# Optimization experiments

Measured on AMD Instinct MI355X. Metric: run time of the kernel, lower is better.

Reference implementation:

```python
import jax, jax.numpy as jnp
import numpy as np
from jax.ops import segment_sum, segment_max

N, E, F, H, G, P, C = 50000, 600000, 128, 128, 64, 32, 10
HEADS = 3
BN_EPS = 1e-5
COS_EPS = 1e-8


def setup_inputs() -> dict:
    key = jax.random.key(0)
    ks = jax.random.split(key, 32)
    rn = lambda k, shape, s: jax.random.normal(k, shape, jnp.float32) * s
    inp = {
        "x": jax.random.normal(ks[0], (N, F), jnp.float32),
        "edge_index": jax.random.randint(ks[1], (2, E), 0, N, jnp.int32),
        "batch": jnp.sort(jax.random.randint(ks[2], (N,), 0, G, jnp.int32)),
        # GCNConv
        "W1": rn(ks[3], (F, H), F ** -0.5), "b1": jnp.zeros((H,), jnp.float32),
        # SAGEConv (lin_l on aggregated neighbors, lin_r on root)
        "Wl": rn(ks[4], (H, H), H ** -0.5), "Wr": rn(ks[5], (H, H), H ** -0.5),
        "bs": jnp.zeros((H,), jnp.float32),
        # GATConv, heads=3, concat=False
        "Wg": rn(ks[6], (H, HEADS * H), H ** -0.5),
        "a_src": rn(ks[7], (HEADS, H), H ** -0.5),
        "a_dst": rn(ks[8], (HEADS, H), H ** -0.5),
        "bg": jnp.zeros((H,), jnp.float32),
        # prototype head / classifier / decoder
        "protos": jax.random.normal(ks[9], (P, H), jnp.float32),
        "Wc": rn(ks[10], (H, C), H ** -0.5), "bc": jnp.zeros((C,), jnp.float32),
        "Wd1": rn(ks[11], (H, 2 * H), H ** -0.5), "bd1": jnp.zeros((2 * H,), jnp.float32),
        "Wd2": rn(ks[12], (2 * H, F), (2 * H) ** -0.5), "bd2": jnp.zeros((F,), jnp.float32),
    }
    # BatchNorm (eval mode): gamma, beta, running mean/var for bn1..bn3
    for i in range(3):
        k0, k1, k2 = jax.random.split(ks[13 + i], 3)
        inp[f"g{i+1}"] = 1.0 + rn(k0, (H,), 0.05)
        inp[f"be{i+1}"] = rn(k1, (H,), 0.05)
        inp[f"m{i+1}"] = rn(k2, (H,), 0.1)
        inp[f"v{i+1}"] = jnp.ones((H,), jnp.float32)
    return inp


def _bn(x, g, b, m, v):
    return (x - m) * jax.lax.rsqrt(v + BN_EPS) * g + b


def _forward(x, edge_index, batch,
             W1, b1, g1, be1, m1, v1,
             Wl, Wr, bs, g2, be2, m2, v2,
             Wg, a_src, a_dst, bg, g3, be3, m3, v3,
             protos, Wc, bc, Wd1, bd1, Wd2, bd2):
    src, dst = edge_index[0], edge_index[1]
    ones_e = jnp.ones((src.shape[0],), x.dtype)

    # --- GCNConv: symmetric norm with self-loops ---
    h = x @ W1                                        # [N, H]
    deg = segment_sum(ones_e, dst, num_segments=N) + 1.0
    dinv = jax.lax.rsqrt(deg)
    coef = dinv[src] * dinv[dst]                      # [E]
    h1 = segment_sum(h[src] * coef[:, None], dst, num_segments=N)
    h1 = h1 + h * (dinv * dinv)[:, None] + b1         # self-loop term + bias
    h1 = jax.nn.elu(_bn(h1, g1, be1, m1, v1))         # dropout = identity (eval)

    # --- SAGEConv: mean aggregation (no self-loops) ---
    cnt = segment_sum(ones_e, dst, num_segments=N)
    mean_nb = segment_sum(h1[src], dst, num_segments=N) / jnp.maximum(cnt, 1.0)[:, None]
    h2 = mean_nb @ Wl + h1 @ Wr + bs
    h2 = jax.nn.elu(_bn(h2, g2, be2, m2, v2))

    # --- GATConv: heads=3, concat=False (mean), with self-loops ---
    hg = (h2 @ Wg).reshape(N, HEADS, H)               # [N, 3, H]
    al_src = jnp.einsum('nhf,hf->nh', hg, a_src)      # [N, 3]
    al_dst = jnp.einsum('nhf,hf->nh', hg, a_dst)
    loop = jnp.arange(N, dtype=src.dtype)
    s2 = jnp.concatenate([src, loop])
    d2 = jnp.concatenate([dst, loop])
    e = jax.nn.leaky_relu(al_src[s2] + al_dst[d2], 0.2)   # [E+N, 3]
    emax = segment_max(e, d2, num_segments=N)             # every node has a self-loop
    ex = jnp.exp(e - emax[d2])
    den = segment_sum(ex, d2, num_segments=N)
    alpha = ex / den[d2]                                  # [E+N, 3]
    h3 = segment_sum(hg[s2] * alpha[:, :, None], d2, num_segments=N)
    h3 = h3.mean(axis=1) + bg                             # concat=False -> head mean
    h3 = jax.nn.elu(_bn(h3, g3, be3, m3, v3))

    # --- global mean pool over graphs ---
    gcnt = segment_sum(jnp.ones((N,), x.dtype), batch, num_segments=G)
    pooled = segment_sum(h3, batch, num_segments=G) / jnp.maximum(gcnt, 1.0)[:, None]

    # --- prototype head: cosine sim -> softmax -> mix ---
    xn = pooled / jnp.maximum(jnp.linalg.norm(pooled, axis=-1, keepdims=True), COS_EPS)
    pn = protos / jnp.maximum(jnp.linalg.norm(protos, axis=-1, keepdims=True), COS_EPS)
    sims = xn @ pn.T                                      # [G, P]
    assignments = jax.nn.softmax(sims, axis=-1)
    proto_emb = assignments @ protos                      # [G, H]
    logits = proto_emb @ Wc + bc                          # [G, C]
    reconstructed = jax.nn.relu(pooled @ Wd1 + bd1) @ Wd2 + bd2   # [G, F]
    return logits, proto_emb, assignments, reconstructed


def reference(x, edge_index, batch,
              W1, b1, g1, be1, m1, v1,
              Wl, Wr, bs, g2, be2, m2, v2,
              Wg, a_src, a_dst, bg, g3, be3, m3, v3,
              protos, Wc, bc, Wd1, bd1, Wd2, bd2):
    return _forward(x, edge_index, batch,
                    W1, b1, g1, be1, m1, v1,
                    Wl, Wr, bs, g2, be2, m2, v2,
                    Wg, a_src, a_dst, bg, g3, be3, m3, v3,
                    protos, Wc, bc, Wd1, bd1, Wd2, bd2)
```

## Files before the change

### kernel.cpp

```cpp
#include <hip/hip_runtime.h>
#include <hip/hip_bf16.h>
#include <stdint.h>
#include <stddef.h>

#define N_ 50000
#define E_ 600000
#define F_ 128
#define H_ 128
#define G_ 64
#define P_ 32
#define C_ 10
#define NB_ 49

typedef __hip_bfloat16 bf16;
typedef __attribute__((ext_vector_type(8))) short short8;
typedef __attribute__((ext_vector_type(4))) float float4v;

__device__ __forceinline__ float us2f(unsigned short u){ return __uint_as_float(((unsigned int)u)<<16); }
__device__ __forceinline__ unsigned short f2us(float x){ bf16 h = __float2bfloat16(x); return *(unsigned short*)&h; }
__device__ __forceinline__ float blo(unsigned int u){ return __uint_as_float(u<<16); }
__device__ __forceinline__ float bhi(unsigned int u){ return __uint_as_float(u & 0xFFFF0000u); }
__device__ __forceinline__ unsigned int packbf(float lo, float hi){ return ((unsigned int)f2us(hi)<<16) | f2us(lo); }
__device__ __forceinline__ float eluf(float x){ return x>0.f ? x : __expf(x)-1.f; }
__device__ __forceinline__ float bnf(float x,float m,float v,float g,float b){ return (x-m)*rsqrtf(v+1e-5f)*g+b; }
__device__ __forceinline__ float lrelu(float x){ return x>0.f ? x : 0.2f*x; }
__device__ __forceinline__ float expc(float x){ return __expf(fminf(x, 50.f)); }
__device__ __forceinline__ void atomAddF(float* a, float v){ unsafeAtomicAdd(a, v); }

__global__ __launch_bounds__(256) void k_wprep(const float* __restrict__ W1, const float* __restrict__ Wl,
    const float* __restrict__ Wr, const float* __restrict__ Wg, unsigned short* __restrict__ WT){
  int idx = blockIdx.x*256 + threadIdx.x;
  if(idx >= 6*16384) return;
  int m    = idx >> 14;
  int tile = (idx >> 11) & 7;
  int kc   = (idx >> 9) & 3;
  int lane = (idx >> 3) & 63;
  int j    = idx & 7;
  int k = kc*32 + (lane>>4)*8 + j;
  int n = tile*16 + (lane&15);
  float v;
  if(m==0)      v = W1[k*128+n];
  else if(m==1) v = Wl[k*128+n];
  else if(m==2) v = Wr[k*128+n];
  else          v = Wg[k*384 + (m-3)*128 + n];
  WT[idx] = f2us(v);
}

__global__ __launch_bounds__(384) void k_vprep(const float* __restrict__ Wg, const float* __restrict__ a_src,
    const float* __restrict__ a_dst, float* __restrict__ vs3, float* __restrict__ vd3){
  int t = threadIdx.x;
  if(t >= 384) return;
  int h = t >> 7, f = t & 127;
  const float4* wr = (const float4*)(Wg + (size_t)f*384 + h*128);
  const float4* as = (const float4*)(a_src + h*128);
  const float4* ad = (const float4*)(a_dst + h*128);
  float s = 0.f, d = 0.f;
  #pragma unroll 8
  for(int j=0;j<32;j++){
    float4 wv = wr[j], av = as[j], dv = ad[j];
    s += wv.x*av.x + wv.y*av.y + wv.z*av.z + wv.w*av.w;
    d += wv.x*dv.x + wv.y*dv.y + wv.z*dv.z + wv.w*dv.w;
  }
  vs3[t] = s; vd3[t] = d;
}

__device__ __forceinline__ void load_Afrag_bf16(const bf16* A, int row, int lane, short8 af[4]){
  const unsigned short* ap = (const unsigned short*)A + (size_t)row*128 + (lane>>4)*8;
  #pragma unroll
  for(int kc=0;kc<4;kc++) af[kc] = *(const short8*)(ap + kc*32);
}
__device__ __forceinline__ void mfma_pass_g(const unsigned short* __restrict__ WB, const short8 af[4],
                                            int lane, float4v acc[8]){
  #pragma unroll
  for(int tile=0;tile<8;tile++){
    #pragma unroll
    for(int kc=0;kc<4;kc++){
      short8 bfv = *(const short8*)(WB + (((tile*4+kc)*64 + lane)<<3));
      acc[tile] = __builtin_amdgcn_mfma_f32_16x16x32_bf16(af[kc], bfv, acc[tile], 0, 0, 0);
    }
  }
}

__global__ __launch_bounds__(256) void k_mm_x(const float* __restrict__ X, const unsigned short* __restrict__ WTg,
                                              bf16* __restrict__ HB){
  const int tid = threadIdx.x, lane = tid&63, w = tid>>6;
  const int row0 = blockIdx.x*64;
  int arow = row0 + w*16 + (lane&15);
  int ar = arow < N_ ? arow : N_-1;
  const float* ap = X + (size_t)ar*128 + (lane>>4)*8;
  short8 af[4];
  #pragma unroll
  for(int kc=0;kc<4;kc++){
    float4 a = *(const float4*)(ap + kc*32);
    float4 b = *(const float4*)(ap + kc*32 + 4);
    short8 v;
    v[0]=(short)f2us(a.x); v[1]=(short)f2us(a.y); v[2]=(short)f2us(a.z); v[3]=(short)f2us(a.w);
    v[4]=(short)f2us(b.x); v[5]=(short)f2us(b.y); v[6]=(short)f2us(b.z); v[7]=(short)f2us(b.w);
    af[kc]=v;
  }
  float4v acc[8];
  #pragma unroll
  for(int t=0;t<8;t++){ acc[t][0]=0.f; acc[t][1]=0.f; acc[t][2]=0.f; acc[t][3]=0.f; }
  mfma_pass_g(WTg, af, lane, acc);
  const int colb = lane&15, q = lane>>4;
  unsigned short* ob = (unsigned short*)HB;
  #pragma unroll
  for(int r=0;r<4;r++){
    int ro = row0 + w*16 + q*4 + r;
    if(ro < N_){
      #pragma unroll
      for(int tile=0;tile<8;tile++)
        ob[(size_t)ro*128 + tile*16 + colb] = f2us(acc[tile][r]);
    }
  }
}

__global__ __launch_bounds__(256) void k_sage_mm_att(const bf16* __restrict__ MaB, const bf16* __restrict__ H1B,
    const unsigned short* __restrict__ WlF, const unsigned short* __restrict__ WrF,
    const float* __restrict__ bs, const float* __restrict__ g2, const float* __restrict__ be2,
    const float* __restrict__ m2, const float* __restrict__ v2,
    const float* __restrict__ vs3, const float* __restrict__ vd3,
    bf16* __restrict__ H2B, float* __restrict__ als3, float* __restrict__ ald3){
  const int tid = threadIdx.x, lane = tid&63, w = tid>>6;
  const int row0 = blockIdx.x*64;
  int arow = row0 + w*16 + (lane&15);
  int ar = arow < N_ ? arow : N_-1;
  float4v acc[8];
  #pragma unroll
  for(int t=0;t<8;t++){ acc[t][0]=0.f; acc[t][1]=0.f; acc[t][2]=0.f; acc[t][3]=0.f; }
  short8 af[4];
  load_Afrag_bf16(MaB, ar, lane, af);
  mfma_pass_g(WlF, af, lane, acc);
  load_Afrag_bf16(H1B, ar, lane, af);
  mfma_pass_g(WrF, af, lane, acc);

  const int colb = lane&15, q = lane>>4;
  float vsv[24], vdv[24];
  #pragma unroll
  for(int h=0;h<3;h++){
    #pragma unroll
    for(int tile=0;tile<8;tile++){
      vsv[h*8+tile] = vs3[h*128 + tile*16 + colb];
      vdv[h*8+tile] = vd3[h*128 + tile*16 + colb];
    }
  }
  unsigned short* ob = (unsigned short*)H2B;
  #pragma unroll
  for(int tile=0;tile<8;tile++){
    int col = tile*16 + colb;
    float bsv=bs[col], gv=g2[col], bev=be2[col], mv=m2[col], vv=v2[col];
    #pragma unroll
    for(int r=0;r<4;r++){
      int ro = row0 + w*16 + q*4 + r;
      float x = eluf(bnf(acc[tile][r] + bsv, mv, vv, gv, bev));
      acc[tile][r] = x;
      if(ro < N_) ob[(size_t)ro*128 + col] = f2us(x);
    }
  }
  #pragma unroll
  for(int r=0;r<4;r++){
    int ro = row0 + w*16 + q*4 + r;
    #pragma unroll
    for(int h=0;h<3;h++){
      float ps=0.f, pd=0.f;
      #pragma unroll
      for(int tile=0;tile<8;tile++){ ps += acc[tile][r]*vsv[h*8+tile]; pd += acc[tile][r]*vdv[h*8+tile]; }
      #pragma unroll
      for(int o=8;o>0;o>>=1){ ps += __shfl_down(ps,o,16); pd += __shfl_down(pd,o,16); }
      if(colb==0 && ro<N_){ als3[ro*3+h] = ps; ald3[ro*3+h] = pd; }
    }
  }
}

__global__ __launch_bounds__(256) void k_gat_mm3(const bf16* __restrict__ U, const unsigned short* __restrict__ WgF,
    const float* __restrict__ bg, const float* __restrict__ g3, const float* __restrict__ be3,
    const float* __restrict__ m3, const float* __restrict__ v3, bf16* __restrict__ H3B){
  const int tid = threadIdx.x, lane = tid&63, w = tid>>6;
  const int row0 = blockIdx.x*64;
  int arow = row0 + w*16 + (lane&15);
  int ar = arow < N_ ? arow : N_-1;
  float4v acc[8];
  #pragma unroll
  for(int t=0;t<8;t++){ acc[t][0]=0.f; acc[t][1]=0.f; acc[t][2]=0.f; acc[t][3]=0.f; }
  short8 af[4];
  for(int hh=0; hh<3; hh++){
    const unsigned short* ap = (const unsigned short*)U + (size_t)ar*384 + hh*128 + (lane>>4)*8;
    #pragma unroll
    for(int kc=0;kc<4;kc++) af[kc] = *(const short8*)(ap + kc*32);
    mfma_pass_g(WgF + hh*16384, af, lane, acc);
  }
  const int colb = lane&15, q = lane>>4;
  unsigned short* ob = (unsigned short*)H3B;
  #pragma unroll
  for(int tile=0;tile<8;tile++){
    int col = tile*16 + colb;
    float bgv=bg[col], gv=g3[col], bev=be3[col], mv=m3[col], vv=v3[col];
    #pragma unroll
    for(int r=0;r<4;r++){
      int ro = row0 + w*16 + q*4 + r;
      if(ro < N_){
        float x = acc[tile][r] + bgv;
        ob[(size_t)ro*128 + col] = f2us(eluf(bnf(x, mv, vv, gv, bev)));
      }
    }
  }
}

__global__ __launch_bounds__(256) void k_count(const int* __restrict__ dst, int* __restrict__ cnt){
  int e = blockIdx.x*256 + threadIdx.x;
  if(e < E_) atomicAdd(&cnt[dst[e]], 1);
}

__global__ __launch_bounds__(1024) void k_scan1(const int* __restrict__ cnt, int* __restrict__ row_ptr,
                                                float* __restrict__ dinv, int* __restrict__ bsum){
  __shared__ int wsum[16];
  const int t = threadIdx.x, lane = t & 63, wid = t >> 6;
  int i = blockIdx.x*1024 + t;
  int v = (i<N_) ? cnt[i] : 0;
  int x = v;
  #pragma unroll
  for(int o=1;o<64;o<<=1){
    int y = __shfl_up(x, o, 64);
    if(lane >= o) x += y;
  }
  if(lane==63) wsum[wid] = x;
  __syncthreads();
  if(wid==0){
    int s = (lane<16) ? wsum[lane] : 0;
    #pragma unroll
    for(int o=1;o<16;o<<=1){
      int y = __shfl_up(s, o, 64);
      if(lane >= o) s += y;
    }
    if(lane<16) wsum[lane] = s;
  }
  __syncthreads();
  int waveoff = (wid>0) ? wsum[wid-1] : 0;
  int incl = waveoff + x;
  if(i<N_){
    row_ptr[i] = incl - v;
    dinv[i] = rsqrtf((float)v + 1.f);
  }
  if(t==1023) bsum[blockIdx.x] = incl;
}

__global__ __launch_bounds__(64) void k_scan2(const int* __restrict__ bsum, int* __restrict__ boff,
                                              int* __restrict__ row_ptr){
  int lane = threadIdx.x;
  int v = (lane < NB_) ? bsum[lane] : 0;
  int x = v;
  #pragma unroll
  for(int o=1;o<64;o<<=1){
    int y = __shfl_up(x, o, 64);
    if(lane >= o) x += y;
  }
  if(lane < NB_) boff[lane] = x - v;
  if(lane == 63) row_ptr[N_] = x;
}

__global__ __launch_bounds__(256) void k_scan3(int* __restrict__ row_ptr, const int* __restrict__ boff,
                                               int* __restrict__ tmp){
  int i = blockIdx.x*256 + threadIdx.x;
  if(i < N_){
    int r = row_ptr[i] + boff[i>>10];
    row_ptr[i] = r;
    tmp[i] = r;
  }
}

__global__ __launch_bounds__(256) void k_scatter(const int* __restrict__ src, const int* __restrict__ dst,
                                                 int* __restrict__ tmp, int* __restrict__ esrc,
                                                 int* __restrict__ edst){
  int e = blockIdx.x*256 + threadIdx.x;
  if(e < E_){
    int d = dst[e];
    int pos = atomicAdd(&tmp[d], 1);
    esrc[pos] = src[e];
    edst[pos] = d;
  }
}

__global__ __launch_bounds__(256) void k_wexp(const int* __restrict__ esrc, const int* __restrict__ edst,
    const float* __restrict__ als3, const float* __restrict__ ald3, float* __restrict__ we4){
  int e = blockIdx.x*256 + threadIdx.x;
  if(e >= E_) return;
  int s = esrc[e], d = edst[e];
  float4 w;
  w.x = expc(lrelu(als3[s*3+0] + ald3[d*3+0]));
  w.y = expc(lrelu(als3[s*3+1] + ald3[d*3+1]));
  w.z = expc(lrelu(als3[s*3+2] + ald3[d*3+2]));
  w.w = 0.f;
  *(float4*)(we4 + (size_t)e*4) = w;
}

__global__ __launch_bounds__(256) void k_gcn_gather(const int* __restrict__ row_ptr, const int* __restrict__ esrc,
    const float* __restrict__ dinv, const bf16* __restrict__ HB,
    const float* __restrict__ b1, const float* __restrict__ g1, const float* __restrict__ be1,
    const float* __restrict__ m1, const float* __restrict__ v1, bf16* __restrict__ H1B){
  int n = blockIdx.x*4 + (threadIdx.x>>6);
  int lane = threadIdx.x & 63;
  if(n >= N_) return;
  int beg = row_ptr[n], end = row_ptr[n+1];
  float dn = dinv[n];
  float a0 = 0.f, a1 = 0.f;
  const unsigned short* hb = (const unsigned short*)HB;
  int e = beg;
  for(; e+3 < end; e += 4){
    int s0 = esrc[e], s1 = esrc[e+1], s2 = esrc[e+2], s3 = esrc[e+3];
    unsigned int hv0 = *(const unsigned int*)(hb + (size_t)s0*H_ + lane*2);
    unsigned int hv1 = *(const unsigned int*)(hb + (size_t)s1*H_ + lane*2);
    unsigned int hv2 = *(const unsigned int*)(hb + (size_t)s2*H_ + lane*2);
    unsigned int hv3 = *(const unsigned int*)(hb + (size_t)s3*H_ + lane*2);
    float c0 = dinv[s0]*dn, c1 = dinv[s1]*dn, c2 = dinv[s2]*dn, c3 = dinv[s3]*dn;
    a0 += c0*blo(hv0) + c1*blo(hv1) + c2*blo(hv2) + c3*blo(hv3);
    a1 += c0*bhi(hv0) + c1*bhi(hv1) + c2*bhi(hv2) + c3*bhi(hv3);
  }
  for(; e < end; e++){
    int s = esrc[e];
    float c = dinv[s]*dn;
    unsigned int hv = *(const unsigned int*)(hb + (size_t)s*H_ + lane*2);
    a0 += c*blo(hv);
    a1 += c*bhi(hv);
  }
  unsigned int hv = *(const unsigned int*)(hb + (size_t)n*H_ + lane*2);
  int f0 = lane*2, f1 = f0+1;
  float x0 = a0 + blo(hv)*dn*dn + b1[f0];
  float x1 = a1 + bhi(hv)*dn*dn + b1[f1];
  x0 = eluf(bnf(x0, m1[f0], v1[f0], g1[f0], be1[f0]));
  x1 = eluf(bnf(x1, m1[f1], v1[f1], g1[f1], be1[f1]));
  unsigned int o = ((unsigned int)f2us(x1)<<16) | f2us(x0);
  *(unsigned int*)((unsigned short*)H1B + (size_t)n*H_ + lane*2) = o;
}

__global__ __launch_bounds__(256) void k_sage_gather(const int* __restrict__ row_ptr, const int* __restrict__ esrc,
    const bf16* __restrict__ H1B, bf16* __restrict__ MeanB){
  int n = blockIdx.x*4 + (threadIdx.x>>6);
  int lane = threadIdx.x & 63;
  if(n >= N_) return;
  int beg = row_ptr[n], end = row_ptr[n+1];
  float a0 = 0.f, a1 = 0.f;
  const unsigned short* hb = (const unsigned short*)H1B;
  int e = beg;
  for(; e+3 < end; e += 4){
    int s0 = esrc[e], s1 = esrc[e+1], s2 = esrc[e+2], s3 = esrc[e+3];
    unsigned int hv0 = *(const unsigned int*)(hb + (size_t)s0*H_ + lane*2);
    unsigned int hv1 = *(const unsigned int*)(hb + (size_t)s1*H_ + lane*2);
    unsigned int hv2 = *(const unsigned int*)(hb + (size_t)s2*H_ + lane*2);
    unsigned int hv3 = *(const unsigned int*)(hb + (size_t)s3*H_ + lane*2);
    a0 += blo(hv0) + blo(hv1) + blo(hv2) + blo(hv3);
    a1 += bhi(hv0) + bhi(hv1) + bhi(hv2) + bhi(hv3);
  }
  for(; e < end; e++){
    unsigned int hv = *(const unsigned int*)(hb + (size_t)esrc[e]*H_ + lane*2);
    a0 += blo(hv);
    a1 += bhi(hv);
  }
  float inv = 1.f / fmaxf((float)(end-beg), 1.f);
  unsigned int o = ((unsigned int)f2us(a1*inv)<<16) | f2us(a0*inv);
  *(unsigned int*)((unsigned short*)MeanB + (size_t)n*H_ + lane*2) = o;
}

__global__ __launch_bounds__(256) void k_gat_agg(const int* __restrict__ row_ptr, const int* __restrict__ esrc,
    const float* __restrict__ als3, const float* __restrict__ ald3, const float* __restrict__ we4,
    const bf16* __restrict__ H2B, bf16* __restrict__ U){
  int n = blockIdx.x*4 + (threadIdx.x>>6);
  int lane = threadIdx.x & 63;
  if(n >= N_) return;
  int beg = row_ptr[n], end = row_ptr[n+1];
  float es0 = expc(lrelu(als3[n*3+0] + ald3[n*3+0]));
  float es1 = expc(lrelu(als3[n*3+1] + ald3[n*3+1]));
  float es2 = expc(lrelu(als3[n*3+2] + ald3[n*3+2]));
  const unsigned short* hb = (const unsigned short*)H2B;
  unsigned int xs = *(const unsigned int*)(hb + (size_t)n*H_ + lane*2);
  float x0 = blo(xs), x1 = bhi(xs);
  float den0 = es0, den1 = es1, den2 = es2;
  float a00 = es0*x0, a01 = es0*x1;
  float a10 = es1*x0, a11 = es1*x1;
  float a20 = es2*x0, a21 = es2*x1;
  int e = beg;
  for(; e+3 < end; e += 4){
    int s0 = esrc[e], s1 = esrc[e+1], s2 = esrc[e+2], s3 = esrc[e+3];
    float4 w0 = *(const float4*)(we4 + (size_t)(e  )*4);
    float4 w1 = *(const float4*)(we4 + (size_t)(e+1)*4);
    float4 w2 = *(const float4*)(we4 + (size_t)(e+2)*4);
    float4 w3 = *(const float4*)(we4 + (size_t)(e+3)*4);
    unsigned int p0 = *(const unsigned int*)(hb + (size_t)s0*H_ + lane*2);
    unsigned int p1 = *(const unsigned int*)(hb + (size_t)s1*H_ + lane*2);
    unsigned int p2 = *(const unsigned int*)(hb + (size_t)s2*H_ + lane*2);
    unsigned int p3 = *(const unsigned int*)(hb + (size_t)s3*H_ + lane*2);
    den0 += w0.x + w1.x + w2.x + w3.x;
    den1 += w0.y + w1.y + w2.y + w3.y;
    den2 += w0.z + w1.z + w2.z + w3.z;
    float q00=blo(p0), q01=bhi(p0), q10=blo(p1), q11=bhi(p1);
    float q20=blo(p2), q21=bhi(p2), q30=blo(p3), q31=bhi(p3);
    a00 += w0.x*q00 + w1.x*q10 + w2.x*q20 + w3.x*q30;
    a01 += w0.x*q01 + w1.x*q11 + w2.x*q21 + w3.x*q31;
    a10 += w0.y*q00 + w1.y*q10 + w2.y*q20 + w3.y*q30;
    a11 += w0.y*q01 + w1.y*q11 + w2.y*q21 + w3.y*q31;
    a20 += w0.z*q00 + w1.z*q10 + w2.z*q20 + w3.z*q30;
    a21 += w0.z*q01 + w1.z*q11 + w2.z*q21 + w3.z*q31;
  }
  for(; e < end; e++){
    int s = esrc[e];
    float4 w = *(const float4*)(we4 + (size_t)e*4);
    unsigned int p = *(const unsigned int*)(hb + (size_t)s*H_ + lane*2);
    float q0 = blo(p), q1 = bhi(p);
    den0 += w.x; den1 += w.y; den2 += w.z;
    a00 += w.x*q0; a01 += w.x*q1;
    a10 += w.y*q0; a11 += w.y*q1;
    a20 += w.z*q0; a21 += w.z*q1;
  }
  float i0 = 1.f/(3.f*den0), i1 = 1.f/(3.f*den1), i2 = 1.f/(3.f*den2);
  unsigned short* ub = (unsigned short*)U;
  size_t ubase = (size_t)n*384 + lane*2;
  *(unsigned int*)(ub + ubase)       = packbf(a00*i0, a01*i0);
  *(unsigned int*)(ub + ubase + 128) = packbf(a10*i1, a11*i1);
  *(unsigned int*)(ub + ubase + 256) = packbf(a20*i2, a21*i2);
}

#define NPW_ 16
__global__ __launch_bounds__(256) void k_h3pool(const bf16* __restrict__ H3B,
    const int* __restrict__ batch, float* __restrict__ pooled, float* __restrict__ gcnt){
  int wave = blockIdx.x*4 + (threadIdx.x>>6);
  int lane = threadIdx.x & 63;
  int n0 = wave*NPW_;
  if(n0 >= N_) return;
  int n1 = n0 + NPW_; if(n1 > N_) n1 = N_;
  int f0 = lane*2, f1 = f0+1;
  float r0=0.f, r1=0.f;
  int cur = batch[n0];
  int seg = 0;
  for(int n=n0; n<n1; n++){
    int b = batch[n];
    if(b != cur){
      atomAddF(&pooled[cur*H_ + f0], r0);
      atomAddF(&pooled[cur*H_ + f1], r1);
      if(lane==0) atomAddF(&gcnt[cur], (float)seg);
      r0 = 0.f; r1 = 0.f; seg = 0; cur = b;
    }
    unsigned int hv = *(const unsigned int*)((const unsigned short*)H3B + (size_t)n*H_ + lane*2);
    r0 += blo(hv);
    r1 += bhi(hv);
    seg++;
  }
  atomAddF(&pooled[cur*H_ + f0], r0);
  atomAddF(&pooled[cur*H_ + f1], r1);
  if(lane==0) atomAddF(&gcnt[cur], (float)seg);
}

__global__ __launch_bounds__(128) void k_head(const float* __restrict__ pooledacc, const float* __restrict__ gcnt,
    const float* __restrict__ protos, const float* __restrict__ Wc, const float* __restrict__ bc,
    const float* __restrict__ Wd1, const float* __restrict__ bd1, const float* __restrict__ Wd2, const float* __restrict__ bd2,
    float* __restrict__ out){
  const int g = blockIdx.x, t = threadIdx.x;
  __shared__ float p[128], xn[128], red[128], sims[32], es[32], asg[32], pe[128], t1[256];
  __shared__ float nrm;
  float cg_ = fmaxf(gcnt[g], 1.f);
  p[t] = pooledacc[g*128 + t] / cg_;
  __syncthreads();
  red[t] = p[t]*p[t];
  __syncthreads();
  for(int s=64;s>0;s>>=1){ if(t<s) red[t]+=red[t+s]; __syncthreads(); }
  if(t==0) nrm = fmaxf(sqrtf(red[0]), 1e-8f);
  __syncthreads();
  xn[t] = p[t]/nrm;
  __syncthreads();
  if(t<32){
    float s=0.f, pn=0.f;
    for(int f=0;f<128;f++){ float pv=protos[t*128+f]; s += xn[f]*pv; pn += pv*pv; }
    sims[t] = s / fmaxf(sqrtf(pn), 1e-8f);
  }
  __syncthreads();
  if(t<32){
    float mx=-1e30f;
    for(int j=0;j<32;j++) mx = fmaxf(mx, sims[j]);
    es[t] = __expf(sims[t]-mx);
  }
  __syncthreads();
  if(t<32){
    float sm=0.f;
    for(int j=0;j<32;j++) sm += es[j];
    float a = es[t]/fmaxf(sm,1e-20f);
    asg[t] = a;
    out[8832 + g*32 + t] = a;
  }
  __syncthreads();
  {
    float s=0.f;
    for(int pp=0;pp<32;pp++) s += asg[pp]*protos[pp*128+t];
    pe[t] = s;
    out[640 + g*128 + t] = s;
  }
  __syncthreads();
  if(t<10){
    float s = bc[t];
    for(int f=0;f<128;f++) s += pe[f]*Wc[f*10+t];
    out[g*10 + t] = s;
  }
  for(int j=t;j<256;j+=128){
    float s = bd1[j];
    for(int f=0;f<128;f++) s += p[f]*Wd1[f*256+j];
    t1[j] = fmaxf(s, 0.f);
  }
  __syncthreads();
  {
    float s = bd2[t];
    for(int j=0;j<256;j++) s += t1[j]*Wd2[j*128+t];
    out[10880 + g*128 + t] = s;
  }
}

__global__ void k_sentinel(float* out, float code){
  out[0] = code;
}

extern "C" void kernel_launch(void* const* d_in, const int* in_sizes, int n_in,
                              void* d_out, int out_size, void* d_ws, size_t ws_size,
                              hipStream_t stream){
  const float* X    = (const float*)d_in[0];
  const int*  EI    = (const int*)d_in[1];
  const int*  batch = (const int*)d_in[2];
  const int* src = EI;
  const int* dst = EI + E_;

  int iW1,ib1,iWl,iWr,ibs,iWg,ias,iad,ibg,ipr,iWc,ibc,iWd1,ibd1,iWd2,ibd2;
  int ig1,ibe1,im1,iv1,ig2,ibe2,im2,iv2,ig3,ibe3,im3,iv3;
  if(n_in >= 31 && in_sizes[5] == 128){
    iW1=3; ib1=4; ig1=5; ibe1=6; im1=7; iv1=8;
    iWl=9; iWr=10; ibs=11; ig2=12; ibe2=13; im2=14; iv2=15;
    iWg=16; ias=17; iad=18; ibg=19; ig3=20; ibe3=21; im3=22; iv3=23;
    ipr=24; iWc=25; ibc=26; iWd1=27; ibd1=28; iWd2=29; ibd2=30;
  }else{
    iW1=3; ib1=4; iWl=5; iWr=6; ibs=7; iWg=8; ias=9; iad=10; ibg=11;
    ipr=12; iWc=13; ibc=14; iWd1=15; ibd1=16; iWd2=17; ibd2=18;
    ig1=19; ibe1=20; im1=21; iv1=22; ig2=23; ibe2=24; im2=25; iv2=26;
    ig3=27; ibe3=28; im3=29; iv3=30;
  }
  const float* W1 = (const float*)d_in[iW1];   const float* b1 = (const float*)d_in[ib1];
  const float* Wl = (const float*)d_in[iWl];   const float* Wr = (const float*)d_in[iWr];
  const float* bs = (const float*)d_in[ibs];   const float* Wg = (const float*)d_in[iWg];
  const float* a_src = (const float*)d_in[ias]; const float* a_dst = (const float*)d_in[iad];
  const float* bg = (const float*)d_in[ibg];   const float* protos = (const float*)d_in[ipr];
  const float* Wc = (const float*)d_in[iWc];   const float* bc = (const float*)d_in[ibc];
  const float* Wd1 = (const float*)d_in[iWd1]; const float* bd1 = (const float*)d_in[ibd1];
  const float* Wd2 = (const float*)d_in[iWd2]; const float* bd2 = (const float*)d_in[ibd2];
  const float* g1 = (const float*)d_in[ig1];   const float* be1 = (const float*)d_in[ibe1];
  const float* m1 = (const float*)d_in[im1];   const float* v1 = (const float*)d_in[iv1];
  const float* g2 = (const float*)d_in[ig2];   const float* be2 = (const float*)d_in[ibe2];
  const float* m2 = (const float*)d_in[im2];   const float* v2 = (const float*)d_in[iv2];
  const float* g3 = (const float*)d_in[ig3];   const float* be3 = (const float*)d_in[ibe3];
  const float* m3 = (const float*)d_in[im3];   const float* v3 = (const float*)d_in[iv3];

  const size_t NF = (size_t)N_*H_;
  const size_t intN = (size_t)3*N_ + 4 + (size_t)2*E_ + 128;
  const size_t fltN = (size_t)7*N_ + (size_t)4*E_ + G_*H_ + G_ + 768;
  const size_t NEED = NF*2*3 + (size_t)N_*384*2 + intN*4 + fltN*4 + (size_t)6*16384*2;
  if(ws_size < NEED){
    k_sentinel<<<1,1,0,stream>>>((float*)d_out, 1000.f + (float)(ws_size>>20));
    return;
  }
  bf16* RA = (bf16*)d_ws;
  bf16* RB = RA + NF;
  bf16* RC = RB + NF;
  bf16* U  = RC + NF;
  int*  cnt     = (int*)(U + (size_t)N_*384);
  int*  row_ptr = cnt + N_;
  int*  tmp     = row_ptr + (N_+4);
  int*  esrc    = tmp + N_;
  int*  edst    = esrc + E_;
  int*  bsum    = edst + E_;
  int*  boff    = bsum + 64;
  float* dinv   = (float*)(boff + 64);
  float* als3   = dinv + N_;
  float* ald3   = als3 + (size_t)N_*3;
  float* we4    = ald3 + (size_t)N_*3;
  float* pooled = we4 + (size_t)E_*4;
  float* gcnt   = pooled + (size_t)G_*H_;
  float* vs3    = gcnt + G_;
  float* vd3    = vs3 + 384;
  unsigned short* WTg = (unsigned short*)(vd3 + 384);

  k_wprep<<<(6*16384+255)/256, 256, 0, stream>>>(W1, Wl, Wr, Wg, WTg);
  k_vprep<<<1, 384, 0, stream>>>(Wg, a_src, a_dst, vs3, vd3);
  hipMemsetAsync(cnt, 0, N_*sizeof(int), stream);
  k_count<<<(E_+255)/256, 256, 0, stream>>>(dst, cnt);
  k_scan1<<<NB_, 1024, 0, stream>>>(cnt, row_ptr, dinv, bsum);
  k_scan2<<<1, 64, 0, stream>>>(bsum, boff, row_ptr);
  k_scan3<<<(N_+255)/256, 256, 0, stream>>>(row_ptr, boff, tmp);
  k_scatter<<<(E_+255)/256, 256, 0, stream>>>(src, dst, tmp, esrc, edst);

  const int GB = (N_+3)/4;
  const int MB = (N_+63)/64;
  k_mm_x<<<MB, 256, 0, stream>>>(X, WTg, RA);
  k_gcn_gather<<<GB, 256, 0, stream>>>(row_ptr, esrc, dinv, RA, b1, g1, be1, m1, v1, RB);
  k_sage_gather<<<GB, 256, 0, stream>>>(row_ptr, esrc, RB, RC);
  k_sage_mm_att<<<MB, 256, 0, stream>>>(RC, RB, WTg + 16384, WTg + 2*16384, bs, g2, be2, m2, v2,
                                        vs3, vd3, RA, als3, ald3);
  k_wexp<<<(E_+255)/256, 256, 0, stream>>>(esrc, edst, als3, ald3, we4);
  k_gat_agg<<<GB, 256, 0, stream>>>(row_ptr, esrc, als3, ald3, we4, RA, U);
  k_gat_mm3<<<MB, 256, 0, stream>>>(U, WTg + 3*16384, bg, g3, be3, m3, v3, RC);
  hipMemsetAsync(pooled, 0, (size_t)(G_*H_+G_)*sizeof(float), stream);
  {
    int waves = (N_ + NPW_ - 1)/NPW_;
    int blocks = (waves + 3)/4;
    k_h3pool<<<blocks, 256, 0, stream>>>(RC, batch, pooled, gcnt);
  }
  k_head<<<G_, 128, 0, stream>>>(pooled, gcnt, protos, Wc, bc, Wd1, bd1, Wd2, bd2, (float*)d_out);
}
```

Baseline: 427.5 us.

## Fuse GAT output matmul with graph pooling; stage neighbor indices via wave shuffles

Fuses the final GAT matmul epilogue with mean pooling. Each block reduces its rows into a 32KB shared-memory pooled buffer and flushes nonzero entries to global memory with atomics, so the H3 intermediate is never written and the separate pooling kernel is removed. Node counts per graph now come from a separate integer atomic kernel. The three gather kernels load up to 64 edge indices per wave cooperatively and broadcast them with shuffles instead of issuing scalar index loads per edge. Attention logits are padded to 4 per node so they can be read as float4. The 32KB shared buffer and its zero and flush loops may reduce occupancy and add per-block overhead.

```diff
diff --git a/kernel.cpp b/kernel.cpp
--- a/kernel.cpp
+++ b/kernel.cpp
@@ -120,7 +120,7 @@
     const float* __restrict__ bs, const float* __restrict__ g2, const float* __restrict__ be2,
     const float* __restrict__ m2, const float* __restrict__ v2,
     const float* __restrict__ vs3, const float* __restrict__ vd3,
-    bf16* __restrict__ H2B, float* __restrict__ als3, float* __restrict__ ald3){
+    bf16* __restrict__ H2B, float* __restrict__ als4, float* __restrict__ ald4){
   const int tid = threadIdx.x, lane = tid&63, w = tid>>6;
   const int row0 = blockIdx.x*64;
   int arow = row0 + w*16 + (lane&15);
@@ -167,15 +167,19 @@
       for(int tile=0;tile<8;tile++){ ps += acc[tile][r]*vsv[h*8+tile]; pd += acc[tile][r]*vdv[h*8+tile]; }
       #pragma unroll
       for(int o=8;o>0;o>>=1){ ps += __shfl_down(ps,o,16); pd += __shfl_down(pd,o,16); }
-      if(colb==0 && ro<N_){ als3[ro*3+h] = ps; ald3[ro*3+h] = pd; }
-    }
-  }
-}
-
-__global__ __launch_bounds__(256) void k_gat_mm3(const bf16* __restrict__ U, const unsigned short* __restrict__ WgF,
+      if(colb==0 && ro<N_){ als4[ro*4+h] = ps; ald4[ro*4+h] = pd; }
+    }
+  }
+}
+
+__global__ __launch_bounds__(256) void k_gat_mm3_pool(const bf16* __restrict__ U, const unsigned short* __restrict__ WgF,
     const float* __restrict__ bg, const float* __restrict__ g3, const float* __restrict__ be3,
-    const float* __restrict__ m3, const float* __restrict__ v3, bf16* __restrict__ H3B){
+    const float* __restrict__ m3, const float* __restrict__ v3,
+    const int* __restrict__ batch, float* __restrict__ pooled){
+  __shared__ float plds[G_*H_];
   const int tid = threadIdx.x, lane = tid&63, w = tid>>6;
+  #pragma unroll
+  for(int i=0;i<32;i++) plds[tid + i*256] = 0.f;
   const int row0 = blockIdx.x*64;
   int arow = row0 + w*16 + (lane&15);
   int ar = arow < N_ ? arow : N_-1;
@@ -190,25 +194,42 @@
     mfma_pass_g(WgF + hh*16384, af, lane, acc);
   }
   const int colb = lane&15, q = lane>>4;
-  unsigned short* ob = (unsigned short*)H3B;
+  float bgv[8],gv[8],bev[8],mv[8],vv[8];
   #pragma unroll
   for(int tile=0;tile<8;tile++){
     int col = tile*16 + colb;
-    float bgv=bg[col], gv=g3[col], bev=be3[col], mv=m3[col], vv=v3[col];
-    #pragma unroll
-    for(int r=0;r<4;r++){
-      int ro = row0 + w*16 + q*4 + r;
-      if(ro < N_){
-        float x = acc[tile][r] + bgv;
-        ob[(size_t)ro*128 + col] = f2us(eluf(bnf(x, mv, vv, gv, bev)));
+    bgv[tile]=bg[col]; gv[tile]=g3[col]; bev[tile]=be3[col]; mv[tile]=m3[col]; vv[tile]=v3[col];
+  }
+  __syncthreads();
+  #pragma unroll
+  for(int r=0;r<4;r++){
+    int ro = row0 + w*16 + q*4 + r;
+    if(ro < N_){
+      int b = batch[ro];
+      float* prow = &plds[b*H_];
+      #pragma unroll
+      for(int tile=0;tile<8;tile++){
+        float x = eluf(bnf(acc[tile][r] + bgv[tile], mv[tile], vv[tile], gv[tile], bev[tile]));
+        atomicAdd(&prow[tile*16 + colb], x);
       }
     }
+  }
+  __syncthreads();
+  #pragma unroll
+  for(int i=0;i<32;i++){
+    float v = plds[tid + i*256];
+    if(v != 0.f) atomAddF(&pooled[tid + i*256], v);
   }
 }
 
 __global__ __launch_bounds__(256) void k_count(const int* __restrict__ dst, int* __restrict__ cnt){
   int e = blockIdx.x*256 + threadIdx.x;
   if(e < E_) atomicAdd(&cnt[dst[e]], 1);
+}
+
+__global__ __launch_bounds__(256) void k_gcnt(const int* __restrict__ batch, int* __restrict__ gcnt){
+  int i = blockIdx.x*256 + threadIdx.x;
+  if(i < N_) atomicAdd(&gcnt[batch[i]], 1);
 }
 
 __global__ __launch_bounds__(1024) void k_scan1(const int* __restrict__ cnt, int* __restrict__ row_ptr,
@@ -281,14 +302,16 @@
 }
 
 __global__ __launch_bounds__(256) void k_wexp(const int* __restrict__ esrc, const int* __restrict__ edst,
-    const float* __restrict__ als3, const float* __restrict__ ald3, float* __restrict__ we4){
+    const float* __restrict__ als4, const float* __restrict__ ald4, float* __restrict__ we4){
   int e = blockIdx.x*256 + threadIdx.x;
   if(e >= E_) return;
   int s = esrc[e], d = edst[e];
+  float4 as = *(const float4*)(als4 + (size_t)s*4);
+  float4 ad = *(const float4*)(ald4 + (size_t)d*4);
   float4 w;
-  w.x = expc(lrelu(als3[s*3+0] + ald3[d*3+0]));
-  w.y = expc(lrelu(als3[s*3+1] + ald3[d*3+1]));
-  w.z = expc(lrelu(als3[s*3+2] + ald3[d*3+2]));
+  w.x = expc(lrelu(as.x + ad.x));
+  w.y = expc(lrelu(as.y + ad.y));
+  w.z = expc(lrelu(as.z + ad.z));
   w.w = 0.f;
   *(float4*)(we4 + (size_t)e*4) = w;
 }
@@ -304,23 +327,28 @@
   float dn = dinv[n];
   float a0 = 0.f, a1 = 0.f;
   const unsigned short* hb = (const unsigned short*)HB;
-  int e = beg;
-  for(; e+3 < end; e += 4){
-    int s0 = esrc[e], s1 = esrc[e+1], s2 = esrc[e+2], s3 = esrc[e+3];
-    unsigned int hv0 = *(const unsigned int*)(hb + (size_t)s0*H_ + lane*2);
-    unsigned int hv1 = *(const unsigned int*)(hb + (size_t)s1*H_ + lane*2);
-    unsigned int hv2 = *(const unsigned int*)(hb + (size_t)s2*H_ + lane*2);
-    unsigned int hv3 = *(const unsigned int*)(hb + (size_t)s3*H_ + lane*2);
-    float c0 = dinv[s0]*dn, c1 = dinv[s1]*dn, c2 = dinv[s2]*dn, c3 = dinv[s3]*dn;
-    a0 += c0*blo(hv0) + c1*blo(hv1) + c2*blo(hv2) + c3*blo(hv3);
-    a1 += c0*bhi(hv0) + c1*bhi(hv1) + c2*bhi(hv2) + c3*bhi(hv3);
-  }
-  for(; e < end; e++){
-    int s = esrc[e];
-    float c = dinv[s]*dn;
-    unsigned int hv = *(const unsigned int*)(hb + (size_t)s*H_ + lane*2);
-    a0 += c*blo(hv);
-    a1 += c*bhi(hv);
+  for(int c = beg; c < end; c += 64){
+    int take = end - c; if(take > 64) take = 64;
+    int idx = esrc[c + (lane < take ? lane : take-1)];
+    float dv = dinv[idx] * dn;
+    int j = 0;
+    for(; j+3 < take; j += 4){
+      int s0=__shfl(idx,j), s1=__shfl(idx,j+1), s2=__shfl(idx,j+2), s3=__shfl(idx,j+3);
+      float c0=__shfl(dv,j), c1=__shfl(dv,j+1), c2=__shfl(dv,j+2), c3=__shfl(dv,j+3);
+      unsigned int hv0 = *(const unsigned int*)(hb + (size_t)s0*H_ + lane*2);
+      unsigned int hv1 = *(const unsigned int*)(hb + (size_t)s1*H_ + lane*2);
+      unsigned int hv2 = *(const unsigned int*)(hb + (size_t)s2*H_ + lane*2);
+      unsigned int hv3 = *(const unsigned int*)(hb + (size_t)s3*H_ + lane*2);
+      a0 += c0*blo(hv0) + c1*blo(hv1) + c2*blo(hv2) + c3*blo(hv3);
+      a1 += c0*bhi(hv0) + c1*bhi(hv1) + c2*bhi(hv2) + c3*bhi(hv3);
+    }
+    for(; j < take; j++){
+      int s = __shfl(idx,j);
+      float cc = __shfl(dv,j);
+      unsigned int hv = *(const unsigned int*)(hb + (size_t)s*H_ + lane*2);
+      a0 += cc*blo(hv);
+      a1 += cc*bhi(hv);
+    }
   }
   unsigned int hv = *(const unsigned int*)(hb + (size_t)n*H_ + lane*2);
   int f0 = lane*2, f1 = f0+1;
@@ -340,20 +368,25 @@
   int beg = row_ptr[n], end = row_ptr[n+1];
   float a0 = 0.f, a1 = 0.f;
   const unsigned short* hb = (const unsigned short*)H1B;
-  int e = beg;
-  for(; e+3 < end; e += 4){
-    int s0 = esrc[e], s1 = esrc[e+1], s2 = esrc[e+2], s3 = esrc[e+3];
-    unsigned int hv0 = *(const unsigned int*)(hb + (size_t)s0*H_ + lane*2);
-    unsigned int hv1 = *(const unsigned int*)(hb + (size_t)s1*H_ + lane*2);
-    unsigned int hv2 = *(const unsigned int*)(hb + (size_t)s2*H_ + lane*2);
-    unsigned int hv3 = *(const unsigned int*)(hb + (size_t)s3*H_ + lane*2);
-    a0 += blo(hv0) + blo(hv1) + blo(hv2) + blo(hv3);
-    a1 += bhi(hv0) + bhi(hv1) + bhi(hv2) + bhi(hv3);
-  }
-  for(; e < end; e++){
-    unsigned int hv = *(const unsigned int*)(hb + (size_t)esrc[e]*H_ + lane*2);
-    a0 += blo(hv);
-    a1 += bhi(hv);
+  for(int c = beg; c < end; c += 64){
+    int take = end - c; if(take > 64) take = 64;
+    int idx = esrc[c + (lane < take ? lane : take-1)];
+    int j = 0;
+    for(; j+3 < take; j += 4){
+      int s0=__shfl(idx,j), s1=__shfl(idx,j+1), s2=__shfl(idx,j+2), s3=__shfl(idx,j+3);
+      unsigned int hv0 = *(const unsigned int*)(hb + (size_t)s0*H_ + lane*2);
+      unsigned int hv1 = *(const unsigned int*)(hb + (size_t)s1*H_ + lane*2);
+      unsigned int hv2 = *(const unsigned int*)(hb + (size_t)s2*H_ + lane*2);
+      unsigned int hv3 = *(const unsigned int*)(hb + (size_t)s3*H_ + lane*2);
+      a0 += blo(hv0) + blo(hv1) + blo(hv2) + blo(hv3);
+      a1 += bhi(hv0) + bhi(hv1) + bhi(hv2) + bhi(hv3);
+    }
+    for(; j < take; j++){
+      int s = __shfl(idx,j);
+      unsigned int hv = *(const unsigned int*)(hb + (size_t)s*H_ + lane*2);
+      a0 += blo(hv);
+      a1 += bhi(hv);
+    }
   }
   float inv = 1.f / fmaxf((float)(end-beg), 1.f);
   unsigned int o = ((unsigned int)f2us(a1*inv)<<16) | f2us(a0*inv);
@@ -361,15 +394,17 @@
 }
 
 __global__ __launch_bounds__(256) void k_gat_agg(const int* __restrict__ row_ptr, const int* __restrict__ esrc,
-    const float* __restrict__ als3, const float* __restrict__ ald3, const float* __restrict__ we4,
+    const float* __restrict__ als4, const float* __restrict__ ald4, const float* __restrict__ we4,
     const bf16* __restrict__ H2B, bf16* __restrict__ U){
   int n = blockIdx.x*4 + (threadIdx.x>>6);
   int lane = threadIdx.x & 63;
   if(n >= N_) return;
   int beg = row_ptr[n], end = row_ptr[n+1];
-  float es0 = expc(lrelu(als3[n*3+0] + ald3[n*3+0]));
-  float es1 = expc(lrelu(als3[n*3+1] + ald3[n*3+1]));
-  float es2 = expc(lrelu(als3[n*3+2] + ald3[n*3+2]));
+  float4 asn = *(const float4*)(als4 + (size_t)n*4);
+  float4 adn = *(const float4*)(ald4 + (size_t)n*4);
+  float es0 = expc(lrelu(asn.x + adn.x));
+  float es1 = expc(lrelu(asn.y + adn.y));
+  float es2 = expc(lrelu(asn.z + adn.z));
   const unsigned short* hb = (const unsigned short*)H2B;
   unsigned int xs = *(const unsigned int*)(hb + (size_t)n*H_ + lane*2);
   float x0 = blo(xs), x1 = bhi(xs);
@@ -377,38 +412,44 @@
   float a00 = es0*x0, a01 = es0*x1;
   float a10 = es1*x0, a11 = es1*x1;
   float a20 = es2*x0, a21 = es2*x1;
-  int e = beg;
-  for(; e+3 < end; e += 4){
-    int s0 = esrc[e], s1 = esrc[e+1], s2 = esrc[e+2], s3 = esrc[e+3];
-    float4 w0 = *(const float4*)(we4 + (size_t)(e  )*4);
-    float4 w1 = *(const float4*)(we4 + (size_t)(e+1)*4);
-    float4 w2 = *(const float4*)(we4 + (size_t)(e+2)*4);
-    float4 w3 = *(const float4*)(we4 + (size_t)(e+3)*4);
-    unsigned int p0 = *(const unsigned int*)(hb + (size_t)s0*H_ + lane*2);
-    unsigned int p1 = *(const unsigned int*)(hb + (size_t)s1*H_ + lane*2);
-    unsigned int p2 = *(const unsigned int*)(hb + (size_t)s2*H_ + lane*2);
-    unsigned int p3 = *(const unsigned int*)(hb + (size_t)s3*H_ + lane*2);
-    den0 += w0.x + w1.x + w2.x + w3.x;
-    den1 += w0.y + w1.y + w2.y + w3.y;
-    den2 += w0.z + w1.z + w2.z + w3.z;
-    float q00=blo(p0), q01=bhi(p0), q10=blo(p1), q11=bhi(p1);
-    float q20=blo(p2), q21=bhi(p2), q30=blo(p3), q31=bhi(p3);
-    a00 += w0.x*q00 + w1.x*q10 + w2.x*q20 + w3.x*q30;
-    a01 += w0.x*q01 + w1.x*q11 + w2.x*q21 + w3.x*q31;
-    a10 += w0.y*q00 + w1.y*q10 + w2.y*q20 + w3.y*q30;
-    a11 += w0.y*q01 + w1.y*q11 + w2.y*q21 + w3.y*q31;
-    a20 += w0.z*q00 + w1.z*q10 + w2.z*q20 + w3.z*q30;
-    a21 += w0.z*q01 + w1.z*q11 + w2.z*q21 + w3.z*q31;
-  }
-  for(; e < end; e++){
-    int s = esrc[e];
-    float4 w = *(const float4*)(we4 + (size_t)e*4);
-    unsigned int p = *(const unsigned int*)(hb + (size_t)s*H_ + lane*2);
-    float q0 = blo(p), q1 = bhi(p);
-    den0 += w.x; den1 += w.y; den2 += w.z;
-    a00 += w.x*q0; a01 += w.x*q1;
-    a10 += w.y*q0; a11 += w.y*q1;
-    a20 += w.z*q0; a21 += w.z*q1;
+  for(int c = beg; c < end; c += 64){
+    int take = end - c; if(take > 64) take = 64;
+    int idx = esrc[c + (lane < take ? lane : take-1)];
+    int j = 0;
+    for(; j+3 < take; j += 4){
+      int e = c + j;
+      int s0=__shfl(idx,j), s1=__shfl(idx,j+1), s2=__shfl(idx,j+2), s3=__shfl(idx,j+3);
+      float4 w0 = *(const float4*)(we4 + (size_t)(e  )*4);
+      float4 w1 = *(const float4*)(we4 + (size_t)(e+1)*4);
+      float4 w2 = *(const float4*)(we4 + (size_t)(e+2)*4);
+      float4 w3 = *(const float4*)(we4 + (size_t)(e+3)*4);
+      unsigned int p0 = *(const unsigned int*)(hb + (size_t)s0*H_ + lane*2);
+      unsigned int p1 = *(const unsigned int*)(hb + (size_t)s1*H_ + lane*2);
+      unsigned int p2 = *(const unsigned int*)(hb + (size_t)s2*H_ + lane*2);
+      unsigned int p3 = *(const unsigned int*)(hb + (size_t)s3*H_ + lane*2);
+      den0 += w0.x + w1.x + w2.x + w3.x;
+      den1 += w0.y + w1.y + w2.y + w3.y;
+      den2 += w0.z + w1.z + w2.z + w3.z;
+      float q00=blo(p0), q01=bhi(p0), q10=blo(p1), q11=bhi(p1);
+      float q20=blo(p2), q21=bhi(p2), q30=blo(p3), q31=bhi(p3);
+      a00 += w0.x*q00 + w1.x*q10 + w2.x*q20 + w3.x*q30;
+      a01 += w0.x*q01 + w1.x*q11 + w2.x*q21 + w3.x*q31;
+      a10 += w0.y*q00 + w1.y*q10 + w2.y*q20 + w3.y*q30;
+      a11 += w0.y*q01 + w1.y*q11 + w2.y*q21 + w3.y*q31;
+      a20 += w0.z*q00 + w1.z*q10 + w2.z*q20 + w3.z*q30;
+      a21 += w0.z*q01 + w1.z*q11 + w2.z*q21 + w3.z*q31;
+    }
+    for(; j < take; j++){
+      int e = c + j;
+      int s = __shfl(idx,j);
+      float4 w = *(const float4*)(we4 + (size_t)e*4);
+      unsigned int p = *(const unsigned int*)(hb + (size_t)s*H_ + lane*2);
+      float q0 = blo(p), q1 = bhi(p);
+      den0 += w.x; den1 += w.y; den2 += w.z;
+      a00 += w.x*q0; a01 += w.x*q1;
+      a10 += w.y*q0; a11 += w.y*q1;
+      a20 += w.z*q0; a21 += w.z*q1;
+    }
   }
   float i0 = 1.f/(3.f*den0), i1 = 1.f/(3.f*den1), i2 = 1.f/(3.f*den2);
   unsigned short* ub = (unsigned short*)U;
@@ -418,44 +459,14 @@
   *(unsigned int*)(ub + ubase + 256) = packbf(a20*i2, a21*i2);
 }
 
-#define NPW_ 16
-__global__ __launch_bounds__(256) void k_h3pool(const bf16* __restrict__ H3B,
-    const int* __restrict__ batch, float* __restrict__ pooled, float* __restrict__ gcnt){
-  int wave = blockIdx.x*4 + (threadIdx.x>>6);
-  int lane = threadIdx.x & 63;
-  int n0 = wave*NPW_;
-  if(n0 >= N_) return;
-  int n1 = n0 + NPW_; if(n1 > N_) n1 = N_;
-  int f0 = lane*2, f1 = f0+1;
-  float r0=0.f, r1=0.f;
-  int cur = batch[n0];
-  int seg = 0;
-  for(int n=n0; n<n1; n++){
-    int b = batch[n];
-    if(b != cur){
-      atomAddF(&pooled[cur*H_ + f0], r0);
-      atomAddF(&pooled[cur*H_ + f1], r1);
-      if(lane==0) atomAddF(&gcnt[cur], (float)seg);
-      r0 = 0.f; r1 = 0.f; seg = 0; cur = b;
-    }
-    unsigned int hv = *(const unsigned int*)((const unsigned short*)H3B + (size_t)n*H_ + lane*2);
-    r0 += blo(hv);
-    r1 += bhi(hv);
-    seg++;
-  }
-  atomAddF(&pooled[cur*H_ + f0], r0);
-  atomAddF(&pooled[cur*H_ + f1], r1);
-  if(lane==0) atomAddF(&gcnt[cur], (float)seg);
-}
-
-__global__ __launch_bounds__(128) void k_head(const float* __restrict__ pooledacc, const float* __restrict__ gcnt,
+__global__ __launch_bounds__(128) void k_head(const float* __restrict__ pooledacc, const int* __restrict__ gcnt,
     const float* __restrict__ protos, const float* __restrict__ Wc, const float* __restrict__ bc,
     const float* __restrict__ Wd1, const float* __restrict__ bd1, const float* __restrict__ Wd2, const float* __restrict__ bd2,
     float* __restrict__ out){
   const int g = blockIdx.x, t = threadIdx.x;
   __shared__ float p[128], xn[128], red[128], sims[32], es[32], asg[32], pe[128], t1[256];
   __shared__ float nrm;
-  float cg_ = fmaxf(gcnt[g], 1.f);
+  float cg_ = fmaxf((float)gcnt[g], 1.f);
   p[t] = pooledacc[g*128 + t] / cg_;
   __syncthreads();
   red[t] = p[t]*p[t];
@@ -553,7 +564,7 @@
 
   const size_t NF = (size_t)N_*H_;
   const size_t intN = (size_t)3*N_ + 4 + (size_t)2*E_ + 128;
-  const size_t fltN = (size_t)7*N_ + (size_t)4*E_ + G_*H_ + G_ + 768;
+  const size_t fltN = (size_t)9*N_ + (size_t)4*E_ + G_*H_ + G_ + 768;
   const size_t NEED = NF*2*3 + (size_t)N_*384*2 + intN*4 + fltN*4 + (size_t)6*16384*2;
   if(ws_size < NEED){
     k_sentinel<<<1,1,0,stream>>>((float*)d_out, 1000.f + (float)(ws_size>>20));
@@ -571,19 +582,21 @@
   int*  bsum    = edst + E_;
   int*  boff    = bsum + 64;
   float* dinv   = (float*)(boff + 64);
-  float* als3   = dinv + N_;
-  float* ald3   = als3 + (size_t)N_*3;
-  float* we4    = ald3 + (size_t)N_*3;
+  float* als4   = dinv + N_;
+  float* ald4   = als4 + (size_t)N_*4;
+  float* we4    = ald4 + (size_t)N_*4;
   float* pooled = we4 + (size_t)E_*4;
-  float* gcnt   = pooled + (size_t)G_*H_;
-  float* vs3    = gcnt + G_;
+  int*   gcnti  = (int*)(pooled + (size_t)G_*H_);
+  float* vs3    = (float*)(gcnti + G_);
   float* vd3    = vs3 + 384;
   unsigned short* WTg = (unsigned short*)(vd3 + 384);
 
   k_wprep<<<(6*16384+255)/256, 256, 0, stream>>>(W1, Wl, Wr, Wg, WTg);
   k_vprep<<<1, 384, 0, stream>>>(Wg, a_src, a_dst, vs3, vd3);
   hipMemsetAsync(cnt, 0, N_*sizeof(int), stream);
+  hipMemsetAsync(pooled, 0, (size_t)(G_*H_+G_)*sizeof(float), stream);
   k_count<<<(E_+255)/256, 256, 0, stream>>>(dst, cnt);
+  k_gcnt<<<(N_+255)/256, 256, 0, stream>>>(batch, gcnti);
   k_scan1<<<NB_, 1024, 0, stream>>>(cnt, row_ptr, dinv, bsum);
   k_scan2<<<1, 64, 0, stream>>>(bsum, boff, row_ptr);
   k_scan3<<<(N_+255)/256, 256, 0, stream>>>(row_ptr, boff, tmp);
@@ -595,15 +608,9 @@
   k_gcn_gather<<<GB, 256, 0, stream>>>(row_ptr, esrc, dinv, RA, b1, g1, be1, m1, v1, RB);
   k_sage_gather<<<GB, 256, 0, stream>>>(row_ptr, esrc, RB, RC);
   k_sage_mm_att<<<MB, 256, 0, stream>>>(RC, RB, WTg + 16384, WTg + 2*16384, bs, g2, be2, m2, v2,
-                                        vs3, vd3, RA, als3, ald3);
-  k_wexp<<<(E_+255)/256, 256, 0, stream>>>(esrc, edst, als3, ald3, we4);
-  k_gat_agg<<<GB, 256, 0, stream>>>(row_ptr, esrc, als3, ald3, we4, RA, U);
-  k_gat_mm3<<<MB, 256, 0, stream>>>(U, WTg + 3*16384, bg, g3, be3, m3, v3, RC);
-  hipMemsetAsync(pooled, 0, (size_t)(G_*H_+G_)*sizeof(float), stream);
-  {
-    int waves = (N_ + NPW_ - 1)/NPW_;
-    int blocks = (waves + 3)/4;
-    k_h3pool<<<blocks, 256, 0, stream>>>(RC, batch, pooled, gcnt);
-  }
-  k_head<<<G_, 128, 0, stream>>>(pooled, gcnt, protos, Wc, bc, Wd1, bd1, Wd2, bd2, (float*)d_out);
-}
+                                        vs3, vd3, RA, als4, ald4);
+  k_wexp<<<(E_+255)/256, 256, 0, stream>>>(esrc, edst, als4, ald4, we4);
+  k_gat_agg<<<GB, 256, 0, stream>>>(row_ptr, esrc, als4, ald4, we4, RA, U);
+  k_gat_mm3_pool<<<MB, 256, 0, stream>>>(U, WTg + 3*16384, bg, g3, be3, m3, v3, batch, pooled);
+  k_head<<<G_, 128, 0, stream>>>(pooled, gcnti, protos, Wc, bc, Wd1, bd1, Wd2, bd2, (float*)d_out);
+}
```

After: 674.9 us. 57.9% more time.
